# Optimization experiments

Measured on AMD Instinct MI355X. Metric: run time of the kernel, lower is better.

The kernel has to match this reference:

```python
import jax, jax.numpy as jnp
import numpy as np

B, S, D, H = 2, 2048, 1024, 16
HD = D // H           # 64
AD = D // 8           # adapter dim 128


def setup_inputs() -> dict:
    key = jax.random.key(0)
    ks = jax.random.split(key, 16)
    s = 1.0 / np.sqrt(D)
    sa = 1.0 / np.sqrt(AD)
    return {
        "q": jax.random.normal(ks[0], (B, S, D), jnp.float32),
        "k": jax.random.normal(ks[1], (B, S, D), jnp.float32),
        "v": jax.random.normal(ks[2], (B, S, D), jnp.float32),
        "Wq": jax.random.normal(ks[3], (D, D), jnp.float32) * s,
        "bq": jnp.zeros((D,), jnp.float32),
        "Wk": jax.random.normal(ks[4], (D, D), jnp.float32) * s,
        "bk": jnp.zeros((D,), jnp.float32),
        "Wv": jax.random.normal(ks[5], (D, D), jnp.float32) * s,
        "bv": jnp.zeros((D,), jnp.float32),
        "Wo": jax.random.normal(ks[6], (D, D), jnp.float32) * s,
        "bo": jnp.zeros((D,), jnp.float32),
        "Wad": jax.random.normal(ks[7], (AD, D), jnp.float32) * s,
        "bad": jnp.zeros((AD,), jnp.float32),
        "Wau": jax.random.normal(ks[8], (D, AD), jnp.float32) * sa,
        "bau": jnp.zeros((D,), jnp.float32),
    }


def reference(q, k, v, Wq, bq, Wk, bk, Wv, bv, Wo, bo, Wad, bad, Wau, bau):
    # Linear projections (torch Linear: x @ W.T + b), split into heads
    def proj(x, W, b):
        y = jnp.einsum('bsd,ed->bse', x, W) + b
        return y.reshape(B, -1, H, HD).transpose(0, 2, 1, 3)  # [B,H,S,HD]

    qh, kh, vh = proj(q, Wq, bq), proj(k, Wk, bk), proj(v, Wv, bv)
    scores = jnp.einsum('bhqd,bhkd->bhqk', qh, kh) / np.sqrt(HD)  # [B,H,S,S]
    attn = jax.nn.softmax(scores, axis=-1)
    ctx = jnp.einsum('bhqk,bhkd->bhqd', attn, vh)
    ctx = ctx.transpose(0, 2, 1, 3).reshape(B, -1, D)  # [B,S,D]
    out = jnp.einsum('bsd,ed->bse', ctx, Wo) + bo
    # adapter: down -> GELU (exact erf) -> up, fused with residual
    a = jnp.einsum('bsd,ad->bsa', out, Wad) + bad
    a = jax.nn.gelu(a, approximate=False)
    a = jnp.einsum('bsa,da->bsd', a, Wau) + bau
    return out + a
```

## Files before the change

kernel.cpp:

```cpp
#include <hip/hip_runtime.h>
#include <hip/hip_bf16.h>
#include <math.h>

typedef __attribute__((ext_vector_type(8))) short short8;
typedef __attribute__((ext_vector_type(4))) float f32x4;

#define MFMA16(a,b,c) __builtin_amdgcn_mfma_f32_16x16x32_bf16((a),(b),(c),0,0,0)

__device__ __forceinline__ unsigned short f2bf(float f){
    union { __hip_bfloat16 b; unsigned short u; } cv;
    cv.b = __float2bfloat16(f);
    return cv.u;
}
__device__ __forceinline__ unsigned pk_bf16(float a, float b){
    unsigned r;
    asm("v_cvt_pk_bf16_f32 %0, %1, %2" : "=v"(r) : "v"(a), "v"(b));
    return r;
}
__device__ __forceinline__ float ex2(float x){
    return __builtin_amdgcn_exp2f(x);
}

#define GLD_LDS16(g, s) \
    __builtin_amdgcn_global_load_lds((const __attribute__((address_space(1))) void*)(g), \
                                     (__attribute__((address_space(3))) void*)(s), 16, 0, 0)

#define QSCALE 0.18033688011112042f
#define DEFER_THR 11.0f

struct CvtJobs {
    const float* src[6];
    unsigned short* dst[6];
    float scale[6];
    int n[6];
};

__global__ __launch_bounds__(256)
void convert_kernel(CvtJobs j, long long total4) {
    long long i4 = (long long)blockIdx.x * blockDim.x + threadIdx.x;
    if (i4 >= total4) return;
    long long rem = i4 * 4;
    int job = 0;
    while (job < 6 && rem >= j.n[job]) { rem -= j.n[job]; ++job; }
    if (job >= 6) return;
    const float sc = j.scale[job];
    const float4 v = *(const float4*)(j.src[job] + rem);
    ushort4 o;
    o.x = f2bf(v.x * sc); o.y = f2bf(v.y * sc);
    o.z = f2bf(v.z * sc); o.w = f2bf(v.w * sc);
    *(ushort4*)(j.dst[job] + rem) = o;
}

struct QKVArgs {
    const float* A[3];
    const unsigned short* W[3];
    const float* bias[3];
    float bscale[3];
    unsigned short* out[3];
};

__global__ __launch_bounds__(256)
void gemm_qkv(QKVArgs ar, int M, int N, int K)
{
    __shared__ unsigned short As[2][128 * 32];
    __shared__ unsigned short Bs[2][128 * 32];

    const int z = blockIdx.z;
    const float* A = ar.A[z];
    const unsigned short* W = ar.W[z];
    const int tid = threadIdx.x;
    const int w = tid >> 6, l = tid & 63;
    const int lr = l & 15, lg = l >> 4;
    const int wr = w >> 1, wc = w & 1;
    const int m0 = blockIdx.x * 128, n0 = blockIdx.y * 128;
    const int ru = lg ^ ((lr >> 1) & 3);

    int arow[4], aslot[4];
    #pragma unroll
    for (int c = 0; c < 4; ++c) {
        const int sid = c * 256 + tid;
        arow[c] = sid >> 3;
        aslot[c] = sid & 7;
    }

    float4 areg[4];
    auto LOADA = [&](int k0) {
        #pragma unroll
        for (int c = 0; c < 4; ++c)
            areg[c] = *(const float4*)((const char*)A +
                        ((size_t)(m0 + arow[c]) * K + k0) * 4 + aslot[c] * 16);
    };
    auto WRITEA = [&](int bf) {
        #pragma unroll
        for (int c = 0; c < 4; ++c) {
            uint2 pk;
            pk.x = pk_bf16(areg[c].x, areg[c].y);
            pk.y = pk_bf16(areg[c].z, areg[c].w);
            const int row = arow[c], s = aslot[c];
            *(uint2*)((char*)&As[bf][0] + row * 64 +
                      (((s >> 1) ^ ((row >> 1) & 3)) * 16) + (s & 1) * 8) = pk;
        }
    };
    auto STAGE_B = [&](int bf, int k0) {
        #pragma unroll
        for (int c = 0; c < 2; ++c) {
            const int cid = c * 256 + tid;
            const int row = cid >> 2, u = cid & 3;
            const int su = u ^ ((row >> 1) & 3);
            GLD_LDS16((const char*)W + ((size_t)(n0 + row) * K + k0) * 2 + su * 16,
                      (char*)&Bs[bf][0] + (c * 256 + w * 64) * 16);
        }
    };

    f32x4 acc[4][4] = {};
    LOADA(0);
    STAGE_B(0, 0);
    WRITEA(0);
    __syncthreads();
    int cur = 0;

    for (int k0 = 0; k0 < K; k0 += 32) {
        const bool more = (k0 + 32 < K);
        if (more) { LOADA(k0 + 32); STAGE_B(cur ^ 1, k0 + 32); }

        short8 af[4], bfr[4];
        #pragma unroll
        for (int i = 0; i < 4; ++i)
            af[i] = *(const short8*)((const char*)&As[cur][0] + (wr * 64 + i * 16 + lr) * 64 + ru * 16);
        #pragma unroll
        for (int jj = 0; jj < 4; ++jj)
            bfr[jj] = *(const short8*)((const char*)&Bs[cur][0] + (wc * 64 + jj * 16 + lr) * 64 + ru * 16);
        #pragma unroll
        for (int i = 0; i < 4; ++i)
            #pragma unroll
            for (int jj = 0; jj < 4; ++jj)
                acc[i][jj] = MFMA16(af[i], bfr[jj], acc[i][jj]);

        if (more) WRITEA(cur ^ 1);
        __syncthreads();
        cur ^= 1;
    }

    const float* bias = ar.bias[z];
    const float bsc = ar.bscale[z];
    unsigned short* out = ar.out[z];
    #pragma unroll
    for (int i = 0; i < 4; ++i)
        #pragma unroll
        for (int jj = 0; jj < 4; ++jj)
            #pragma unroll
            for (int r = 0; r < 4; ++r) {
                const int row = m0 + wr * 64 + i * 16 + lg * 4 + r;
                const int col = n0 + wc * 64 + jj * 16 + lr;
                const float c = acc[i][jj][r] + bias[col] * bsc;
                const int b = row >> 11, s = row & 2047, h = col >> 6, hd = col & 63;
                if (z < 2)
                    out[((((size_t)(b * 16 + h)) * 2048 + s) << 6) + hd] = f2bf(c);
                else
                    out[((((size_t)(b * 16 + h)) * 64 + hd) << 11) + s] = f2bf(c);
            }
}

template<int MODE>
__global__ __launch_bounds__(256)
void gemm_bf16(const unsigned short* __restrict__ A,
               const unsigned short* __restrict__ Wt,
               const float* __restrict__ bias,
               void* __restrict__ out0,
               void* __restrict__ out1,
               int M, int N, int K)
{
    __shared__ unsigned short As[2][128 * 32];
    __shared__ unsigned short Bs[2][128 * 32];

    const int tid = threadIdx.x;
    const int w = tid >> 6, l = tid & 63;
    const int lr = l & 15, lg = l >> 4;
    const int wr = w >> 1, wc = w & 1;
    const int m0 = blockIdx.x * 128, n0 = blockIdx.y * 128;
    const int ru = lg ^ ((lr >> 1) & 3);

    auto STAGE = [&](int bf, int k0) {
        #pragma unroll
        for (int c = 0; c < 2; ++c) {
            const int cid = c * 256 + tid;
            const int row = cid >> 2, u = cid & 3;
            const int su = u ^ ((row >> 1) & 3);
            GLD_LDS16((const char*)A  + ((size_t)(m0 + row) * K + k0) * 2 + su * 16,
                      (char*)&As[bf][0] + (c * 256 + w * 64) * 16);
            GLD_LDS16((const char*)Wt + ((size_t)(n0 + row) * K + k0) * 2 + su * 16,
                      (char*)&Bs[bf][0] + (c * 256 + w * 64) * 16);
        }
    };

    f32x4 acc[4][4] = {};
    STAGE(0, 0);
    __syncthreads();
    int cur = 0;

    for (int k0 = 0; k0 < K; k0 += 32) {
        if (k0 + 32 < K) STAGE(cur ^ 1, k0 + 32);

        short8 af[4], bfr[4];
        #pragma unroll
        for (int i = 0; i < 4; ++i)
            af[i] = *(const short8*)((const char*)&As[cur][0] + (wr * 64 + i * 16 + lr) * 64 + ru * 16);
        #pragma unroll
        for (int jj = 0; jj < 4; ++jj)
            bfr[jj] = *(const short8*)((const char*)&Bs[cur][0] + (wc * 64 + jj * 16 + lr) * 64 + ru * 16);
        #pragma unroll
        for (int i = 0; i < 4; ++i)
            #pragma unroll
            for (int jj = 0; jj < 4; ++jj)
                acc[i][jj] = MFMA16(af[i], bfr[jj], acc[i][jj]);

        __syncthreads();
        cur ^= 1;
    }

    #pragma unroll
    for (int i = 0; i < 4; ++i)
        #pragma unroll
        for (int jj = 0; jj < 4; ++jj)
            #pragma unroll
            for (int r = 0; r < 4; ++r) {
                const int row = m0 + wr * 64 + i * 16 + lg * 4 + r;
                const int col = n0 + wc * 64 + jj * 16 + lr;
                const float c = acc[i][jj][r] + bias[col];
                if (MODE == 2) {
                    ((float*)out0)[(size_t)row * N + col] = c;
                    ((unsigned short*)out1)[(size_t)row * N + col] = f2bf(c);
                } else {
                    ((float*)out0)[(size_t)row * N + col] =
                        c + ((const float*)out1)[(size_t)row * N + col];
                }
            }
}

__global__ __launch_bounds__(256)
void gemm64_gelu(const unsigned short* __restrict__ A,
                 const unsigned short* __restrict__ Wt,
                 const float* __restrict__ bias,
                 unsigned short* __restrict__ out,
                 int M, int N, int K)
{
    __shared__ unsigned short As[2][64 * 32];
    __shared__ unsigned short Bs[2][64 * 32];

    const int tid = threadIdx.x;
    const int w = tid >> 6, l = tid & 63;
    const int lr = l & 15, lg = l >> 4;
    const int wr = w >> 1, wc = w & 1;
    const int m0 = blockIdx.x * 64, n0 = blockIdx.y * 64;

    auto STAGE = [&](int bf, int k0) {
        const int row = tid >> 2, ch = tid & 3;
        GLD_LDS16(A  + (size_t)(m0 + row) * K + k0 + ch * 8, &As[bf][0] + (w * 64) * 8);
        GLD_LDS16(Wt + (size_t)(n0 + row) * K + k0 + ch * 8, &Bs[bf][0] + (w * 64) * 8);
    };

    f32x4 acc[2][2] = {};
    STAGE(0, 0);
    __syncthreads();
    int cur = 0;

    for (int k0 = 0; k0 < K; k0 += 32) {
        if (k0 + 32 < K) STAGE(cur ^ 1, k0 + 32);

        short8 af[2], bfr[2];
        #pragma unroll
        for (int i = 0; i < 2; ++i)
            af[i] = *(const short8*)(&As[cur][0] + ((wr * 32 + i * 16 + lr) * 32 + lg * 8));
        #pragma unroll
        for (int jj = 0; jj < 2; ++jj)
            bfr[jj] = *(const short8*)(&Bs[cur][0] + ((wc * 32 + jj * 16 + lr) * 32 + lg * 8));
        #pragma unroll
        for (int i = 0; i < 2; ++i)
            #pragma unroll
            for (int jj = 0; jj < 2; ++jj)
                acc[i][jj] = MFMA16(af[i], bfr[jj], acc[i][jj]);

        __syncthreads();
        cur ^= 1;
    }

    #pragma unroll
    for (int i = 0; i < 2; ++i)
        #pragma unroll
        for (int jj = 0; jj < 2; ++jj)
            #pragma unroll
            for (int r = 0; r < 4; ++r) {
                const int row = m0 + wr * 32 + i * 16 + lg * 4 + r;
                const int col = n0 + wc * 32 + jj * 16 + lr;
                const float c = acc[i][jj][r] + bias[col];
                const float g = 0.5f * c * (1.0f + erff(c * 0.70710678118654752f));
                out[(size_t)row * N + col] = f2bf(g);
            }
}

__global__ __launch_bounds__(512)
void attn_mfma(const unsigned short* __restrict__ Qh,
               const unsigned short* __restrict__ Kh,
               const unsigned short* __restrict__ Vt,
               unsigned short* __restrict__ ctx)
{
    __shared__ unsigned short Ks[2][64 * 64];
    __shared__ unsigned short Vs[2][64 * 64];
    __shared__ unsigned short Ps[8][16 * 64];

    const int tid = threadIdx.x;
    const int w = tid >> 6, l = tid & 63;
    const int lr = l & 15, lg = l >> 4;

    const int p = blockIdx.x + blockIdx.y * 16;
    const int id = (p & 7) * 64 + (p >> 3);
    const int q0 = (id & 15) << 7;
    const int bh = id >> 4;

    const unsigned short* Qb = Qh + (size_t)bh * 131072;
    const char* Kb = (const char*)(Kh + (size_t)bh * 131072);
    const char* Vb = (const char*)(Vt + (size_t)bh * 131072);

    short8 qf[2];
    #pragma unroll
    for (int c = 0; c < 2; ++c)
        qf[c] = *(const short8*)(Qb + (size_t)(q0 + w * 16 + lr) * 64 + c * 32 + lg * 8);

    float mrow = -1e30f;
    float lrow = 0.f;
    f32x4 accO[4] = {};

    auto STAGE = [&](int bf, int kt) {
        const int row = tid >> 3, u = tid & 7;
        const int su = u ^ (row & 7);
        GLD_LDS16(Kb + (size_t)(kt + row) * 128 + su * 16,
                  (char*)&Ks[bf][0] + (w * 64) * 16);
        GLD_LDS16(Vb + (size_t)row * 4096 + (size_t)kt * 2 + su * 16,
                  (char*)&Vs[bf][0] + (w * 64) * 16);
    };

    STAGE(0, 0);
    __syncthreads();

    int cur = 0;
    for (int t = 0; t < 32; ++t) {
        if (t < 31) STAGE(cur ^ 1, (t + 1) * 64);

        const char* Kbuf = (const char*)&Ks[cur][0];
        const char* Vbuf = (const char*)&Vs[cur][0];

        f32x4 sf[4] = {};
        __builtin_amdgcn_s_setprio(1);
        #pragma unroll
        for (int n = 0; n < 4; ++n) {
            const int krow = n * 16 + lr;
            const short8 kf0 = *(const short8*)(Kbuf + krow * 128 + ((0 * 4 + lg) ^ (lr & 7)) * 16);
            const short8 kf1 = *(const short8*)(Kbuf + krow * 128 + ((1 * 4 + lg) ^ (lr & 7)) * 16);
            sf[n] = MFMA16(kf0, qf[0], sf[n]);
            sf[n] = MFMA16(kf1, qf[1], sf[n]);
        }
        __builtin_amdgcn_s_setprio(0);

        short8 vf[4][2];
        #pragma unroll
        for (int n = 0; n < 4; ++n) {
            const int drow = n * 16 + lr;
            vf[n][0] = *(const short8*)(Vbuf + drow * 128 + ((0 * 4 + lg) ^ (lr & 7)) * 16);
            vf[n][1] = *(const short8*)(Vbuf + drow * 128 + ((1 * 4 + lg) ^ (lr & 7)) * 16);
        }

        float a = fmaxf(fmaxf(fmaxf(sf[0][0], sf[0][1]), fmaxf(sf[0][2], sf[0][3])),
                        fmaxf(fmaxf(sf[1][0], sf[1][1]), fmaxf(sf[1][2], sf[1][3])));
        float b2 = fmaxf(fmaxf(fmaxf(sf[2][0], sf[2][1]), fmaxf(sf[2][2], sf[2][3])),
                         fmaxf(fmaxf(sf[3][0], sf[3][1]), fmaxf(sf[3][2], sf[3][3])));
        float r2 = fmaxf(a, b2);
        r2 = fmaxf(r2, __shfl_xor(r2, 16));
        r2 = fmaxf(r2, __shfl_xor(r2, 32));
        const bool need = (r2 > mrow + DEFER_THR);
        if (__any(need)) {
            const float mnew = fmaxf(mrow, r2);
            const float rsc = ex2(mrow - mnew);
            lrow *= rsc;
            mrow = mnew;
            #pragma unroll
            for (int r = 0; r < 4; ++r) {
                const float rr = __shfl(rsc, (l & 48) | (lg * 4 + r));
                #pragma unroll
                for (int n = 0; n < 4; ++n) accO[n][r] *= rr;
            }
        }
        {
            const float m = mrow;
            float ls = lrow;
            char* pbase = (char*)&Ps[w][0] + lr * 128;
            #pragma unroll
            for (int n = 0; n < 4; ++n) {
                const float p0 = ex2(sf[n][0] - m);
                const float p1 = ex2(sf[n][1] - m);
                const float p2 = ex2(sf[n][2] - m);
                const float p3 = ex2(sf[n][3] - m);
                ls += (p0 + p1) + (p2 + p3);
                uint2 pk;
                pk.x = pk_bf16(p0, p1);
                pk.y = pk_bf16(p2, p3);
                *(uint2*)(pbase + (((n * 2 + (lg >> 1)) ^ (lr & 7)) * 16) + (lg & 1) * 8) = pk;
            }
            lrow = ls;
        }

        asm volatile("" ::: "memory");

        short8 pf[2];
        {
            const char* pb = (const char*)&Ps[w][0] + lr * 128;
            #pragma unroll
            for (int c = 0; c < 2; ++c) {
                union { uint2 q2[2]; short8 s8; } cvt;
                const char* base = pb + (((c * 4 + lg) ^ (lr & 7)) * 16);
                cvt.q2[0] = *(const uint2*)(base);
                cvt.q2[1] = *(const uint2*)(base + 8);
                pf[c] = cvt.s8;
            }
        }

        __builtin_amdgcn_s_setprio(1);
        #pragma unroll
        for (int n = 0; n < 4; ++n) {
            accO[n] = MFMA16(pf[0], vf[n][0], accO[n]);
            accO[n] = MFMA16(pf[1], vf[n][1], accO[n]);
        }
        __builtin_amdgcn_s_setprio(0);

        __syncthreads();
        cur ^= 1;
    }

    const int b = bh >> 4, h = bh & 15;
    {
        float ls = lrow;
        ls += __shfl_xor(ls, 16);
        ls += __shfl_xor(ls, 32);
        const float inv = 1.0f / ls;
        #pragma unroll
        for (int r = 0; r < 4; ++r) {
            const float vr = __shfl(inv, (l & 48) | (lg * 4 + r));
            const int srow = q0 + w * 16 + lg * 4 + r;
            const size_t base = ((size_t)b * 2048 + srow) * 1024 + h * 64;
            #pragma unroll
            for (int n = 0; n < 4; ++n)
                ctx[base + n * 16 + lr] = f2bf(accO[n][r] * vr);
        }
    }
}

extern "C" void kernel_launch(void* const* d_in, const int* in_sizes, int n_in,
                              void* d_out, int out_size, void* d_ws, size_t ws_size,
                              hipStream_t stream) {
    const float* q   = (const float*)d_in[0];
    const float* k   = (const float*)d_in[1];
    const float* v   = (const float*)d_in[2];
    const float* Wq  = (const float*)d_in[3];
    const float* bq  = (const float*)d_in[4];
    const float* Wk  = (const float*)d_in[5];
    const float* bk  = (const float*)d_in[6];
    const float* Wv  = (const float*)d_in[7];
    const float* bv  = (const float*)d_in[8];
    const float* Wo  = (const float*)d_in[9];
    const float* bo  = (const float*)d_in[10];
    const float* Wad = (const float*)d_in[11];
    const float* bad = (const float*)d_in[12];
    const float* Wau = (const float*)d_in[13];
    const float* bau = (const float*)d_in[14];

    const int M = 4096, D = 1024, AD = 128;
    const size_t SZ = (size_t)M * D;

    char* p = (char*)d_ws;
    size_t off = 0;
    auto alloc = [&](size_t bytes) { void* r = p + off; off = (off + bytes + 255) & ~(size_t)255; return r; };
    unsigned short* Wqb  = (unsigned short*)alloc((size_t)D * D * 2);
    unsigned short* Wkb  = (unsigned short*)alloc((size_t)D * D * 2);
    unsigned short* Wvb  = (unsigned short*)alloc((size_t)D * D * 2);
    unsigned short* Wob  = (unsigned short*)alloc((size_t)D * D * 2);
    unsigned short* Wadb = (unsigned short*)alloc((size_t)AD * D * 2);
    unsigned short* Waub = (unsigned short*)alloc((size_t)D * AD * 2);
    unsigned short* Qh   = (unsigned short*)alloc(SZ * 2);
    unsigned short* Kh   = (unsigned short*)alloc(SZ * 2);
    unsigned short* Vt   = (unsigned short*)alloc(SZ * 2);
    unsigned short* ctx  = (unsigned short*)alloc(SZ * 2);
    float*          outp = (float*)alloc(SZ * 4);
    unsigned short* outb = (unsigned short*)alloc(SZ * 2);
    unsigned short* a1   = (unsigned short*)alloc((size_t)M * AD * 2);

    CvtJobs j;
    j.src[0] = Wq;  j.dst[0] = Wqb;  j.n[0] = D * D;   j.scale[0] = QSCALE;
    j.src[1] = Wk;  j.dst[1] = Wkb;  j.n[1] = D * D;   j.scale[1] = 1.f;
    j.src[2] = Wv;  j.dst[2] = Wvb;  j.n[2] = D * D;   j.scale[2] = 1.f;
    j.src[3] = Wo;  j.dst[3] = Wob;  j.n[3] = D * D;   j.scale[3] = 1.f;
    j.src[4] = Wad; j.dst[4] = Wadb; j.n[4] = AD * D;  j.scale[4] = 1.f;
    j.src[5] = Wau; j.dst[5] = Waub; j.n[5] = D * AD;  j.scale[5] = 1.f;
    long long total = 4LL * D * D + 2LL * AD * D;
    long long total4 = total / 4;
    convert_kernel<<<dim3((unsigned)((total4 + 255) / 256)), dim3(256), 0, stream>>>(j, total4);

    const dim3 blk(256);

    QKVArgs qa;
    qa.A[0] = q;   qa.A[1] = k;   qa.A[2] = v;
    qa.W[0] = Wqb; qa.W[1] = Wkb; qa.W[2] = Wvb;
    qa.bias[0] = bq; qa.bias[1] = bk; qa.bias[2] = bv;
    qa.bscale[0] = QSCALE; qa.bscale[1] = 1.f; qa.bscale[2] = 1.f;
    qa.out[0] = Qh; qa.out[1] = Kh; qa.out[2] = Vt;
    gemm_qkv<<<dim3(M / 128, D / 128, 3), blk, 0, stream>>>(qa, M, D, D);

    attn_mfma<<<dim3(16, 32), dim3(512), 0, stream>>>(Qh, Kh, Vt, ctx);

    gemm_bf16<2><<<dim3(M / 128, D / 128), blk, 0, stream>>>(ctx, Wob, bo, outp, outb, M, D, D);
    gemm64_gelu<<<dim3(M / 64, AD / 64), blk, 0, stream>>>(outb, Wadb, bad, a1, M, AD, D);
    gemm_bf16<4><<<dim3(M / 128, D / 128), blk, 0, stream>>>(a1, Waub, bau, d_out, outp, M, D, AD);
}
```

Before: 152.4 us.

## Prefetch QKV GEMM tiles two stages ahead via register double-buffering

Replaces the direct global-to-LDS load of the weight tile with register loads followed by swizzled LDS stores, and double-buffers both A and B in registers so global loads are issued two k-steps ahead of their use. The main loop is unrolled by two with fixed buffer indices. The aim is to hide global memory latency better behind the MFMA work. In exchange it uses more registers, which may lower occupancy, adds VGPR-to-LDS store traffic for B, and hardcodes K=1024 (32 iterations).

```diff
diff --git a/kernel.cpp b/kernel.cpp
--- a/kernel.cpp
+++ b/kernel.cpp
@@ -75,70 +75,73 @@
     const int m0 = blockIdx.x * 128, n0 = blockIdx.y * 128;
     const int ru = lg ^ ((lr >> 1) & 3);
 
-    int arow[4], aslot[4];
-    #pragma unroll
-    for (int c = 0; c < 4; ++c) {
-        const int sid = c * 256 + tid;
-        arow[c] = sid >> 3;
-        aslot[c] = sid & 7;
-    }
-
-    float4 areg[4];
-    auto LOADA = [&](int k0) {
-        #pragma unroll
-        for (int c = 0; c < 4; ++c)
-            areg[c] = *(const float4*)((const char*)A +
-                        ((size_t)(m0 + arow[c]) * K + k0) * 4 + aslot[c] * 16);
-    };
-    auto WRITEA = [&](int bf) {
+    float4 a0[4], a1[4];
+    int4   b0[2], b1[2];
+
+    auto LOADA = [&](float4* arr, int k0) {
         #pragma unroll
         for (int c = 0; c < 4; ++c) {
+            const int sid = c * 256 + tid, row = sid >> 3, s = sid & 7;
+            arr[c] = *(const float4*)(A + (size_t)(m0 + row) * K + k0 + s * 4);
+        }
+    };
+    auto LOADB = [&](int4* brr, int k0) {
+        #pragma unroll
+        for (int c = 0; c < 2; ++c) {
+            const int cid = c * 256 + tid, row = cid >> 2, u = cid & 3;
+            brr[c] = *(const int4*)(W + (size_t)(n0 + row) * K + k0 + u * 8);
+        }
+    };
+    auto WRITE = [&](const float4* arr, const int4* brr, int bf) {
+        #pragma unroll
+        for (int c = 0; c < 4; ++c) {
+            const int sid = c * 256 + tid, row = sid >> 3, s = sid & 7;
             uint2 pk;
-            pk.x = pk_bf16(areg[c].x, areg[c].y);
-            pk.y = pk_bf16(areg[c].z, areg[c].w);
-            const int row = arow[c], s = aslot[c];
+            pk.x = pk_bf16(arr[c].x, arr[c].y);
+            pk.y = pk_bf16(arr[c].z, arr[c].w);
             *(uint2*)((char*)&As[bf][0] + row * 64 +
                       (((s >> 1) ^ ((row >> 1) & 3)) * 16) + (s & 1) * 8) = pk;
         }
-    };
-    auto STAGE_B = [&](int bf, int k0) {
         #pragma unroll
         for (int c = 0; c < 2; ++c) {
-            const int cid = c * 256 + tid;
-            const int row = cid >> 2, u = cid & 3;
-            const int su = u ^ ((row >> 1) & 3);
-            GLD_LDS16((const char*)W + ((size_t)(n0 + row) * K + k0) * 2 + su * 16,
-                      (char*)&Bs[bf][0] + (c * 256 + w * 64) * 16);
+            const int cid = c * 256 + tid, row = cid >> 2, u = cid & 3;
+            *(int4*)((char*)&Bs[bf][0] + row * 64 +
+                     ((u ^ ((row >> 1) & 3)) * 16)) = brr[c];
         }
     };
 
     f32x4 acc[4][4] = {};
-    LOADA(0);
-    STAGE_B(0, 0);
-    WRITEA(0);
-    __syncthreads();
-    int cur = 0;
-
-    for (int k0 = 0; k0 < K; k0 += 32) {
-        const bool more = (k0 + 32 < K);
-        if (more) { LOADA(k0 + 32); STAGE_B(cur ^ 1, k0 + 32); }
-
+
+    auto COMPUTE = [&](int bf) {
         short8 af[4], bfr[4];
         #pragma unroll
         for (int i = 0; i < 4; ++i)
-            af[i] = *(const short8*)((const char*)&As[cur][0] + (wr * 64 + i * 16 + lr) * 64 + ru * 16);
+            af[i] = *(const short8*)((const char*)&As[bf][0] + (wr * 64 + i * 16 + lr) * 64 + ru * 16);
         #pragma unroll
         for (int jj = 0; jj < 4; ++jj)
-            bfr[jj] = *(const short8*)((const char*)&Bs[cur][0] + (wc * 64 + jj * 16 + lr) * 64 + ru * 16);
+            bfr[jj] = *(const short8*)((const char*)&Bs[bf][0] + (wc * 64 + jj * 16 + lr) * 64 + ru * 16);
         #pragma unroll
         for (int i = 0; i < 4; ++i)
             #pragma unroll
             for (int jj = 0; jj < 4; ++jj)
                 acc[i][jj] = MFMA16(af[i], bfr[jj], acc[i][jj]);
-
-        if (more) WRITEA(cur ^ 1);
+    };
+
+    LOADA(a0, 0);  LOADB(b0, 0);
+    WRITE(a0, b0, 0);
+    LOADA(a1, 32); LOADB(b1, 32);
+    __syncthreads();
+
+    for (int t = 0; t < 32; t += 2) {
+        if (t + 2 < 32) { LOADA(a0, (t + 2) * 32); LOADB(b0, (t + 2) * 32); }
+        COMPUTE(0);
+        if (t + 1 < 32) WRITE(a1, b1, 1);
         __syncthreads();
-        cur ^= 1;
+
+        if (t + 3 < 32) { LOADA(a1, (t + 3) * 32); LOADB(b1, (t + 3) * 32); }
+        COMPUTE(1);
+        if (t + 2 < 32) WRITE(a0, b0, 0);
+        __syncthreads();
     }
 
     const float* bias = ar.bias[z];
```

Measured after the change: 204.5 us. 34.2% more time.
